# Kernel tuning notes

Measured on AMD Instinct MI355X. Metric: run time of the kernel, lower is better.

## Reference

```python
import jax, jax.numpy as jnp
import numpy as np

VOC = 50000
EMB = 300
B = 256
CTX = 6
K = 10


def setup_inputs() -> dict:
    key = jax.random.key(0)
    k1, k2, k3, k4, k5, k6 = jax.random.split(key, 6)
    # one-hot inputs (the original multiplies one-hot vectors against the tables)
    idx_vo = jax.random.randint(k1, (B,), 0, VOC)
    idx_vi = jax.random.randint(k2, (B, CTX), 0, VOC)
    idx_neg = jax.random.randint(k3, (B, K), 0, VOC)
    # random context lengths in [1, CTX]; positions >= length are zero rows (padding)
    lengths = jax.random.randint(k4, (B, 1), 1, CTX + 1)
    valid = (jnp.arange(CTX)[None, :] < lengths).astype(jnp.float32)  # [B, CTX]
    vo = jax.nn.one_hot(idx_vo, VOC, dtype=jnp.float32)               # [B, VOC]
    vi = jax.nn.one_hot(idx_vi, VOC, dtype=jnp.float32) * valid[:, :, None]  # [B, CTX, VOC]
    neg_samples = jax.nn.one_hot(idx_neg, VOC, dtype=jnp.float32)     # [B, K, VOC]
    # parameters: uniform(-0.5, 0.5) / embed_dim, as in the torch init
    V = (jax.random.uniform(k5, (VOC, EMB), minval=-0.5, maxval=0.5) / EMB).astype(jnp.float32)
    U = (jax.random.uniform(k6, (VOC, EMB), minval=-0.5, maxval=0.5) / EMB).astype(jnp.float32)
    return {"vo": vo, "vi": vi, "neg_samples": neg_samples, "V": V, "U": U}


def reference(vo, vi, neg_samples, V, U):
    embed_dim = V.shape[1]
    vo_embed = vo @ V                                      # [B, D]
    vi_temp = jnp.einsum('bcv,vd->bcd', vi, U)             # [B, CTX, D]
    mask = jnp.sum(jnp.abs(vi), axis=2) != 0               # [B, CTX]
    mask_sum = mask.astype(jnp.float32).sum(axis=1, keepdims=True)  # [B, 1]
    vi_embed = vi_temp.sum(axis=1) / mask_sum              # [B, D]
    left = jax.nn.log_sigmoid(jnp.sum(vo_embed * vi_embed, axis=1, keepdims=True))  # [B, 1]
    neg_embed = jnp.einsum('bkv,vd->bkd', neg_samples, U)  # [B, K, D]
    batch_mul = jnp.einsum('bkd,bd->bk', neg_embed, vo_embed)  # [B, K]
    right = jnp.sum(jax.nn.log_sigmoid(-batch_mul), axis=1, keepdims=True)  # [B, 1]
    return jnp.mean(-(left + right))
```

## Files before the change

kernel.cpp:

```cpp
#include <hip/hip_runtime.h>
#include <math.h>

#define VOC 50000
#define EMB 300
#define BSZ 256
#define CTX 6
#define KNEG 10
#define ROW_VECS (VOC / 4)

__global__ void scan_onehot_kernel(const float4* __restrict__ data,
                                   int nvecs,
                                   int* __restrict__ out_idx) {
    int stride = gridDim.x * blockDim.x;
    for (int j = blockIdx.x * blockDim.x + threadIdx.x; j < nvecs; j += stride) {
        float4 v = data[j];
        if (v.x != 0.0f || v.y != 0.0f || v.z != 0.0f || v.w != 0.0f) {
            int row = j / ROW_VECS;
            int col = (j - row * ROW_VECS) * 4;
            if (v.x != 0.0f)      col += 0;
            else if (v.y != 0.0f) col += 1;
            else if (v.z != 0.0f) col += 2;
            else                  col += 3;
            out_idx[row] = col;
        }
    }
}

__device__ __forceinline__ float log_sigmoid(float x) {
    return fminf(x, 0.0f) - log1pf(expf(-fabsf(x)));
}

__global__ void cbow_loss_kernel(const int* __restrict__ idx_vo,
                                 const int* __restrict__ idx_vi,
                                 const int* __restrict__ idx_neg,
                                 const float* __restrict__ V,
                                 const float* __restrict__ U,
                                 float* __restrict__ out) {
    const int b = blockIdx.x;
    const int lane = threadIdx.x;

    float vo_e[5] = {0.f, 0.f, 0.f, 0.f, 0.f};
    float vi_e[5] = {0.f, 0.f, 0.f, 0.f, 0.f};

    const int ivo = idx_vo[b];
    const float* __restrict__ vrow = V + (long)ivo * EMB;
#pragma unroll
    for (int j = 0; j < 5; ++j) {
        int d = lane + j * 64;
        if (d < EMB) vo_e[j] = vrow[d];
    }

    int cnt = 0;
#pragma unroll
    for (int c = 0; c < CTX; ++c) {
        int iv = idx_vi[b * CTX + c];
        if (iv >= 0) {
            ++cnt;
            const float* __restrict__ urow = U + (long)iv * EMB;
#pragma unroll
            for (int j = 0; j < 5; ++j) {
                int d = lane + j * 64;
                if (d < EMB) vi_e[j] += urow[d];
            }
        }
    }
    const float inv_cnt = 1.0f / (float)cnt;

    float dot = 0.f;
#pragma unroll
    for (int j = 0; j < 5; ++j) dot += vo_e[j] * (vi_e[j] * inv_cnt);
#pragma unroll
    for (int off = 32; off > 0; off >>= 1) dot += __shfl_down(dot, off, 64);

    float right = 0.f;
#pragma unroll
    for (int k = 0; k < KNEG; ++k) {
        int in = idx_neg[b * KNEG + k];
        const float* __restrict__ urow = U + (long)in * EMB;
        float pd = 0.f;
#pragma unroll
        for (int j = 0; j < 5; ++j) {
            int d = lane + j * 64;
            if (d < EMB) pd += vo_e[j] * urow[d];
        }
#pragma unroll
        for (int off = 32; off > 0; off >>= 1) pd += __shfl_down(pd, off, 64);
        if (lane == 0) right += log_sigmoid(-pd);
    }

    if (lane == 0) {
        float left = log_sigmoid(dot);
        atomicAdd(out, -(left + right) * (1.0f / (float)BSZ));
    }
}

extern "C" void kernel_launch(void* const* d_in, const int* in_sizes, int n_in,
                              void* d_out, int out_size, void* d_ws, size_t ws_size,
                              hipStream_t stream) {
    const float* vo  = (const float*)d_in[0];
    const float* vi  = (const float*)d_in[1];
    const float* neg = (const float*)d_in[2];
    const float* V   = (const float*)d_in[3];
    const float* U   = (const float*)d_in[4];
    float* out = (float*)d_out;

    int* idx_vo  = (int*)d_ws;
    int* idx_vi  = idx_vo + BSZ;
    int* idx_neg = idx_vi + BSZ * CTX;
    const size_t idx_bytes = (size_t)(BSZ + BSZ * CTX + BSZ * KNEG) * sizeof(int);

    hipMemsetAsync(d_ws, 0xFF, idx_bytes, stream);
    hipMemsetAsync(d_out, 0, sizeof(float), stream);

    const int threads = 256;
    const int scan_blocks = 4096;

    scan_onehot_kernel<<<scan_blocks, threads, 0, stream>>>(
        (const float4*)vo, BSZ * ROW_VECS, idx_vo);
    scan_onehot_kernel<<<scan_blocks, threads, 0, stream>>>(
        (const float4*)vi, BSZ * CTX * ROW_VECS, idx_vi);
    scan_onehot_kernel<<<scan_blocks, threads, 0, stream>>>(
        (const float4*)neg, BSZ * KNEG * ROW_VECS, idx_neg);

    cbow_loss_kernel<<<BSZ, 64, 0, stream>>>(idx_vo, idx_vi, idx_neg, V, U, out);
}
```

Baseline: 936.2 us.

## Scan one-hot rows per block with early exit and fuse scan launches

Replaces three grid-stride scans plus memsets with one kernel that assigns a block per one-hot row and stops reading the row once the nonzero is found. This roughly halves the bytes read for non-padding rows and removes launch and memset overhead. It also uses nontemporal loads and initializes the output in-kernel. Padding rows still require a full scan, and the per-chunk block syncs add some latency.

```diff
diff --git a/kernel.cpp b/kernel.cpp
--- a/kernel.cpp
+++ b/kernel.cpp
@@ -7,23 +7,51 @@
 #define CTX 6
 #define KNEG 10
 #define ROW_VECS (VOC / 4)
+#define NROWS (BSZ + BSZ * CTX + BSZ * KNEG)
 
-__global__ void scan_onehot_kernel(const float4* __restrict__ data,
-                                   int nvecs,
-                                   int* __restrict__ out_idx) {
-    int stride = gridDim.x * blockDim.x;
-    for (int j = blockIdx.x * blockDim.x + threadIdx.x; j < nvecs; j += stride) {
-        float4 v = data[j];
-        if (v.x != 0.0f || v.y != 0.0f || v.z != 0.0f || v.w != 0.0f) {
-            int row = j / ROW_VECS;
-            int col = (j - row * ROW_VECS) * 4;
-            if (v.x != 0.0f)      col += 0;
-            else if (v.y != 0.0f) col += 1;
-            else if (v.z != 0.0f) col += 2;
-            else                  col += 3;
-            out_idx[row] = col;
+typedef float floatx4 __attribute__((ext_vector_type(4)));
+
+__global__ __launch_bounds__(256) void scan_rows_kernel(
+        const floatx4* __restrict__ vo,
+        const floatx4* __restrict__ vi,
+        const floatx4* __restrict__ neg,
+        int* __restrict__ out_idx,
+        float* __restrict__ out) {
+    const int r = blockIdx.x;
+    if (r == 0 && threadIdx.x == 0) *out = 0.0f;
+
+    const floatx4* __restrict__ row;
+    if (r < BSZ)                 row = vo  + (size_t)r * ROW_VECS;
+    else if (r < BSZ + BSZ*CTX)  row = vi  + (size_t)(r - BSZ) * ROW_VECS;
+    else                         row = neg + (size_t)(r - BSZ - BSZ*CTX) * ROW_VECS;
+
+    __shared__ int found;
+    if (threadIdx.x == 0) found = 0;
+    __syncthreads();
+
+    const int t = threadIdx.x;
+    for (int base = 0; base < ROW_VECS; base += 512) {
+#pragma unroll
+        for (int u = 0; u < 2; ++u) {
+            int j = base + u * 256 + t;
+            if (j < ROW_VECS) {
+                floatx4 v = __builtin_nontemporal_load(&row[j]);
+                if (v.x != 0.0f || v.y != 0.0f || v.z != 0.0f || v.w != 0.0f) {
+                    int col = j * 4;
+                    if (v.x != 0.0f)      col += 0;
+                    else if (v.y != 0.0f) col += 1;
+                    else if (v.z != 0.0f) col += 2;
+                    else                  col += 3;
+                    out_idx[r] = col;
+                    found = 1;
+                }
+            }
         }
+        __syncthreads();
+        if (found) return;
+        __syncthreads();
     }
+    if (t == 0) out_idx[r] = -1;
 }
 
 __device__ __forceinline__ float log_sigmoid(float x) {
@@ -104,23 +132,14 @@
     const float* U   = (const float*)d_in[4];
     float* out = (float*)d_out;
 
-    int* idx_vo  = (int*)d_ws;
-    int* idx_vi  = idx_vo + BSZ;
-    int* idx_neg = idx_vi + BSZ * CTX;
-    const size_t idx_bytes = (size_t)(BSZ + BSZ * CTX + BSZ * KNEG) * sizeof(int);
+    int* idx_all = (int*)d_ws;
+    int* idx_vo  = idx_all;
+    int* idx_vi  = idx_all + BSZ;
+    int* idx_neg = idx_all + BSZ + BSZ * CTX;
 
-    hipMemsetAsync(d_ws, 0xFF, idx_bytes, stream);
-    hipMemsetAsync(d_out, 0, sizeof(float), stream);
-
-    const int threads = 256;
-    const int scan_blocks = 4096;
-
-    scan_onehot_kernel<<<scan_blocks, threads, 0, stream>>>(
-        (const float4*)vo, BSZ * ROW_VECS, idx_vo);
-    scan_onehot_kernel<<<scan_blocks, threads, 0, stream>>>(
-        (const float4*)vi, BSZ * CTX * ROW_VECS, idx_vi);
-    scan_onehot_kernel<<<scan_blocks, threads, 0, stream>>>(
-        (const float4*)neg, BSZ * KNEG * ROW_VECS, idx_neg);
+    scan_rows_kernel<<<NROWS, 256, 0, stream>>>(
+        (const floatx4*)vo, (const floatx4*)vi, (const floatx4*)neg,
+        idx_all, out);
 
     cbow_loss_kernel<<<BSZ, 64, 0, stream>>>(idx_vo, idx_vi, idx_neg, V, U, out);
 }
```

Result: faster. 849.6 us (-9.3%).
